# Kernel tuning notes

Measured on AMD Instinct MI355X. Metric: run time of the kernel, lower is better.

The kernel has to match this reference:

```python
import jax, jax.numpy as jnp
import numpy as np

N_NODES = 50000
F_DIM = 256
D_EMB = 128
R_REL = 3
N_PICK = 4096
K_NEIGH = 32


def _dist_score(x, w1, b1, w2, b2):
    # distance_net: Linear(F,16) -> ReLU -> Linear(16,2) -> Sigmoid; take class-1 column
    h = jax.nn.relu(x @ w1 + b1)
    return jax.nn.sigmoid(h @ w2 + b2)[..., 1]


def setup_inputs() -> dict:
    key = jax.random.key(0)
    ks = jax.random.split(key, 10)
    return {
        "features": jax.random.normal(ks[0], (N_NODES, F_DIM), dtype=jnp.float32),
        "weight": jax.random.normal(ks[1], (D_EMB, F_DIM), dtype=jnp.float32) * (1.0 / np.sqrt(F_DIM)),
        "W1": jax.random.normal(ks[2], (R_REL, F_DIM, 16), dtype=jnp.float32) * (1.0 / np.sqrt(F_DIM)),
        "b1": jax.random.normal(ks[3], (R_REL, 16), dtype=jnp.float32) * 0.01,
        "W2": jax.random.normal(ks[4], (R_REL, 16, 2), dtype=jnp.float32) * 0.25,
        "b2": jax.random.normal(ks[5], (R_REL, 2), dtype=jnp.float32) * 0.01,
        "picked_nodes": jax.random.randint(ks[6], (R_REL, N_PICK), 0, N_NODES),
        "picked_labels": jax.random.randint(ks[7], (R_REL, N_PICK), 0, 2),
        "neigh_idx": jax.random.randint(ks[8], (R_REL, N_PICK, K_NEIGH), 0, N_NODES),
        "cand_idx": jax.random.randint(ks[9], (R_REL, N_PICK, K_NEIGH), 0, N_NODES),
    }


def reference(features, weight, W1, b1, W2, b2, picked_nodes, picked_labels, neigh_idx, cand_idx):
    R, n = picked_nodes.shape
    K = neigh_idx.shape[-1]
    dt = features.dtype
    agg = jnp.zeros((n, features.shape[1]), dtype=dt)  # [n, F]
    triu = jnp.triu(jnp.ones((n, n), dtype=dt), 1)
    for r in range(R):  # small fixed relation loop (structurally distinct params)
        lab = picked_labels[r]
        feats_r = features[picked_nodes[r]]                       # [n, F]
        d = _dist_score(feats_r, W1[r], b1[r], W2[r], b2[r])      # [n]
        # ----- rho_plus: top-K mean of pairwise |d_a - d_b| among minority-class nodes -----
        n_pos = jnp.sum(lab)
        minority = jnp.where(n_pos <= n - n_pos, 1, 0)
        minmask = (lab == minority).astype(dt)                    # [n]
        pair = jnp.abs(d[:, None] - d[None, :])                   # [n, n]
        valid = minmask[:, None] * minmask[None, :] * triu
        masked = jnp.where(valid > 0, pair, -1.0)
        top_plus, _ = jax.lax.top_k(masked.reshape(-1), K)        # avg neighborhood size ~ K
        rho_plus = jnp.mean(jnp.maximum(top_plus, 0.0))
        # ----- rho_minus: top n/2 mean of |d_v - d_u| over graph neighbors -----
        nfeat = features[neigh_idx[r]]                            # [n, K, F]
        d_nb = _dist_score(nfeat, W1[r], b1[r], W2[r], b2[r])     # [n, K]
        diff_nb = jnp.abs(d[:, None] - d_nb)                      # [n, K]
        top_minus, _ = jax.lax.top_k(diff_nb.reshape(-1), n // 2)
        rho_minus = jnp.mean(top_minus)
        # ----- gather neighbor features where distance diff below thresholds -----
        m_minus = (diff_nb < rho_minus).astype(dt)                # [n, K]
        cfeat = features[cand_idx[r]]                             # [n, K, F] same-label candidates
        d_cd = _dist_score(cfeat, W1[r], b1[r], W2[r], b2[r])     # [n, K]
        m_plus = (jnp.abs(d[:, None] - d_cd) < rho_plus).astype(dt)
        agg = agg + jnp.einsum('nk,nkf->nf', m_minus, nfeat) + jnp.einsum('nk,nkf->nf', m_plus, cfeat)
    center = features[picked_nodes[0]]                            # [n, F] center batch
    center_h = weight @ center.T                                  # [D, n]
    neigh_h = weight @ agg.T                                      # [D, n]
    return jax.nn.relu(center_h + neigh_h)                        # [D, n]
```

## Files before the change

kernel.cpp:

```cpp
#include <hip/hip_runtime.h>
#include <math.h>

#define NN 50000
#define FD 256
#define DE 128
#define RR 3
#define NP 4096
#define KN 32

#define OFF_DPICK 0
#define OFF_DNB   12288
#define OFF_DCD   405504
#define OFF_RHOM  798720
#define OFF_RHOP  798724
#define OFF_DALL  798976
#define OFF_AGG   798976
#define OFF_HIST  948976
#define OFF_STATE 955120
#define OFF_PSUM  955128
#define OFF_PCNT  955224

__device__ __forceinline__ int wave_red_int(int v) {
    #pragma unroll
    for (int o = 1; o < 64; o <<= 1) v += __shfl_xor(v, o);
    return v;
}
__device__ __forceinline__ double wave_red_dbl(double v) {
    #pragma unroll
    for (int o = 1; o < 64; o <<= 1) v += __shfl_xor(v, o);
    return v;
}

__device__ unsigned kth_bits(const float* arr, int L, int K,
                             int (*cnt_sh)[16], unsigned* x_sh_p) {
    const int tid = threadIdx.x, lane = tid & 63, wv = tid >> 6;
    unsigned x = 0;
    for (int b = 27; b >= 0; b -= 3) {
        int cnt[7];
        #pragma unroll
        for (int q = 0; q < 7; ++q) cnt[q] = 0;
        for (int i = tid; i < L; i += 1024) {
            unsigned vb = __float_as_uint(arr[i]);
            #pragma unroll
            for (int q = 0; q < 7; ++q) cnt[q] += (vb >= (x | ((unsigned)(q + 1) << b)));
        }
        #pragma unroll
        for (int q = 0; q < 7; ++q) cnt[q] = wave_red_int(cnt[q]);
        if (lane == 0) {
            #pragma unroll
            for (int q = 0; q < 7; ++q) cnt_sh[q][wv] = cnt[q];
        }
        __syncthreads();
        if (tid == 0) {
            unsigned nx = x;
            for (int q = 6; q >= 0; --q) {
                int tot = 0;
                for (int w = 0; w < 16; ++w) tot += cnt_sh[q][w];
                if (tot >= K) { nx = x | ((unsigned)(q + 1) << b); break; }
            }
            *x_sh_p = nx;
        }
        __syncthreads();
        x = *x_sh_p;
        __syncthreads();
    }
    return x;
}

__global__ __launch_bounds__(256, 4) void dall_kernel(
    const float* __restrict__ features,
    const float* __restrict__ W1, const float* __restrict__ b1,
    const float* __restrict__ W2, const float* __restrict__ b2,
    float* ws)
{
    const int r = blockIdx.y;
    const int wid = blockIdx.x * 4 + (threadIdx.x >> 6);
    const int lane = threadIdx.x & 63;
    const int s = lane >> 4, j = lane & 15;
    const int base = wid * 32;
    if (base >= NN) return;

    float w1f[64];
    const float* W1r = W1 + r * (FD * 16);
    #pragma unroll
    for (int tt = 0; tt < 64; ++tt) w1f[tt] = W1r[(s * 64 + tt) * 16 + j];
    const float b1v = b1[r * 16 + j];
    const float w2v = W2[(r * 16 + j) * 2 + 1];
    const float b2v = b2[r * 2 + 1];

    float res = 0.f;
    #pragma unroll 2
    for (int i = 0; i < 32; ++i) {
        const int node = min(base + i, NN - 1);
        const float4* x4 = (const float4*)(features + (long)node * FD);
        float acc = 0.f;
        #pragma unroll
        for (int t4 = 0; t4 < 16; ++t4) {
            float4 xv = x4[s * 16 + t4];
            acc = fmaf(xv.x, w1f[4 * t4 + 0], acc);
            acc = fmaf(xv.y, w1f[4 * t4 + 1], acc);
            acc = fmaf(xv.z, w1f[4 * t4 + 2], acc);
            acc = fmaf(xv.w, w1f[4 * t4 + 3], acc);
        }
        acc += __shfl_xor(acc, 16);
        acc += __shfl_xor(acc, 32);
        float h = fmaxf(acc + b1v, 0.f);
        float p = h * w2v;
        p += __shfl_xor(p, 1);
        p += __shfl_xor(p, 2);
        p += __shfl_xor(p, 4);
        p += __shfl_xor(p, 8);
        if (lane == i) res = p;
    }
    const int node = base + lane;
    if (lane < 32 && node < NN)
        ws[OFF_DALL + r * NN + node] = 1.f / (1.f + expf(-(res + b2v)));
}

__global__ __launch_bounds__(256) void gather_kernel(
    const int* __restrict__ picked, const int* __restrict__ neigh,
    const int* __restrict__ cand, float* ws)
{
    const int t = blockIdx.x * 256 + threadIdx.x;
    const float* dall = ws + OFF_DALL;
    if (t < 6144) ((int*)(ws + OFF_HIST))[t] = 0;
    else if (t < 6150) {
        int* st = (int*)(ws + OFF_STATE);
        if (t < 6147) st[t - 6144] = 0;
        else          st[t - 6147 + 3] = NP / 2;
    }
    if (t < RR * NP) {
        const int r = t >> 12;
        ws[OFF_DPICK + t] = dall[r * NN + picked[t]];
    } else if (t < RR * NP + RR * NP * KN) {
        const int off = t - RR * NP;
        const int r = off >> 17;
        const int n = (off >> 5) & (NP - 1);
        const float dp = dall[r * NN + picked[r * NP + n]];
        ws[OFF_DNB + off] = fabsf(dp - dall[r * NN + neigh[off]]);
    } else {
        const int off = t - RR * NP - RR * NP * KN;
        const int r = off >> 17;
        const int n = (off >> 5) & (NP - 1);
        const float dp = dall[r * NN + picked[r * NP + n]];
        ws[OFF_DCD + off] = fabsf(dp - dall[r * NN + cand[off]]);
    }
}

__global__ __launch_bounds__(256) void rho_hist_kernel(float* ws, int pass)
{
    __shared__ int h[4][2048];
    const int tid = threadIdx.x, wv = tid >> 6;
    const int r = blockIdx.y;
    for (int i = tid; i < 8192; i += 256) ((int*)h)[i] = 0;
    __syncthreads();

    const int* st = (const int*)(ws + OFF_STATE);
    const unsigned prefix = (unsigned)st[r];
    const float* __restrict__ dnb = ws + OFF_DNB + r * (NP * KN);
    const int base = blockIdx.x * 8192;
    #pragma unroll 4
    for (int k = 0; k < 32; ++k) {
        unsigned vb = __float_as_uint(dnb[base + k * 256 + tid]);
        int bin; bool ok;
        if (pass == 0)      { bin = vb >> 21;           ok = true; }
        else if (pass == 1) { bin = (vb >> 10) & 0x7FF; ok = ((vb >> 21) == prefix); }
        else                { bin = vb & 0x3FF;         ok = ((vb >> 10) == prefix); }
        if (ok) atomicAdd(&h[wv][bin], 1);
    }
    __syncthreads();
    int* hist = (int*)(ws + OFF_HIST) + r * 2048;
    for (int b = tid; b < 2048; b += 256) {
        int s = h[0][b] + h[1][b] + h[2][b] + h[3][b];
        if (s) atomicAdd(&hist[b], s);
    }
}

__global__ __launch_bounds__(1024) void rho_select_kernel(float* ws, int pass)
{
    __shared__ int s0[2048], s1[2048];
    const int tid = threadIdx.x;
    const int r = blockIdx.x;
    int* hist = (int*)(ws + OFF_HIST) + r * 2048;
    int* st = (int*)(ws + OFF_STATE);

    s0[tid] = hist[tid]; s0[tid + 1024] = hist[tid + 1024];
    __syncthreads();
    int* src = s0; int* dst = s1;
    for (int off = 1; off < 2048; off <<= 1) {
        for (int i = tid; i < 2048; i += 1024) {
            int v = src[i];
            if (i + off < 2048) v += src[i + off];
            dst[i] = v;
        }
        __syncthreads();
        int* tmp = src; src = dst; dst = tmp;
    }
    const int remK = st[3 + r];
    for (int i = tid; i < 2048; i += 1024) {
        const int sfx = src[i];
        const int nxt = (i < 2047) ? src[i + 1] : 0;
        if (sfx >= remK && nxt < remK) {
            const unsigned prefix = (unsigned)st[r];
            st[r] = (pass == 0) ? i
                  : (pass == 1) ? (int)((prefix << 11) | (unsigned)i)
                                : (int)((prefix << 10) | (unsigned)i);
            st[3 + r] = remK - nxt;
        }
        hist[i] = 0;
    }
}

__global__ __launch_bounds__(256) void rho_sum_kernel(float* ws)
{
    __shared__ double ds[4];
    __shared__ int    is[4];
    const int tid = threadIdx.x, lane = tid & 63, wv = tid >> 6;
    const int r = blockIdx.y;
    const unsigned x = (unsigned)((const int*)(ws + OFF_STATE))[r];
    const float* __restrict__ dnb = ws + OFF_DNB + r * (NP * KN);
    const int base = blockIdx.x * 8192;
    double s = 0.0; int c = 0;
    #pragma unroll 4
    for (int k = 0; k < 32; ++k) {
        float v = dnb[base + k * 256 + tid];
        if (__float_as_uint(v) > x) { s += (double)v; c += 1; }
    }
    s = wave_red_dbl(s); c = wave_red_int(c);
    if (lane == 0) { ds[wv] = s; is[wv] = c; }
    __syncthreads();
    if (tid == 0) {
        double st = ds[0] + ds[1] + ds[2] + ds[3];
        int ct = is[0] + is[1] + is[2] + is[3];
        ((double*)(ws + OFF_PSUM))[r * 16 + blockIdx.x] = st;
        ((int*)(ws + OFF_PCNT))[r * 16 + blockIdx.x] = ct;
    }
}

__global__ __launch_bounds__(1024) void rho_plus_kernel(float* ws, const int* __restrict__ labels)
{
    __shared__ float cv[2048];
    __shared__ float cnd[2048];
    __shared__ float tvb[64];
    __shared__ int   cnt_sh[7][16];
    __shared__ int   ired[16];
    __shared__ double dred[16];
    __shared__ int   m_sh, npos_sh, cnt2_sh;
    __shared__ unsigned x_sh;

    const int tid = threadIdx.x;
    const int lane = tid & 63, wv = tid >> 6;
    const int r = blockIdx.x;

    if (tid == 0) {
        const double* psum = (const double*)(ws + OFF_PSUM);
        const int* pcnt = (const int*)(ws + OFF_PCNT);
        double tot = 0; int cg = 0;
        for (int i = 0; i < 16; ++i) { tot += psum[r * 16 + i]; cg += pcnt[r * 16 + i]; }
        const unsigned x = (unsigned)((const int*)(ws + OFF_STATE))[r];
        tot += (double)(NP / 2 - cg) * (double)__uint_as_float(x);
        ws[OFF_RHOM + r] = (float)(tot / (double)(NP / 2));
    }

    const float* dpr = ws + OFF_DPICK + r * NP;
    const int* lab = labels + r * NP;
    int np = 0;
    for (int i = tid; i < NP; i += 1024) np += lab[i];
    np = wave_red_int(np);
    if (lane == 0) ired[wv] = np;
    __syncthreads();
    if (tid == 0) {
        int sacc = 0;
        for (int w = 0; w < 16; ++w) sacc += ired[w];
        npos_sh = sacc; m_sh = 0;
    }
    __syncthreads();
    const int minority = (2 * npos_sh <= NP) ? 1 : 0;
    for (int i = tid; i < NP; i += 1024) {
        bool pred = (lab[i] == minority);
        unsigned long long bal = __ballot(pred);
        int wcnt = __popcll(bal);
        int woff = __popcll(bal & ((1ull << lane) - 1ull));
        int bb = 0;
        if (lane == 0 && wcnt) bb = atomicAdd(&m_sh, wcnt);
        bb = __shfl(bb, 0);
        if (pred) cv[bb + woff] = dpr[i];
    }
    __syncthreads();
    const int m = m_sh;

    if (m >= 64) {
        const unsigned thi = kth_bits(cv, m, 32, cnt_sh, &x_sh);
        if (tid == 0) cnt2_sh = 0;
        __syncthreads();
        for (int i = tid; i < m; i += 1024) {
            bool pred = __float_as_uint(cv[i]) > thi;
            unsigned long long bal = __ballot(pred);
            int wcnt = __popcll(bal);
            int woff = __popcll(bal & ((1ull << lane) - 1ull));
            int bb = 0;
            if (lane == 0 && wcnt) bb = atomicAdd(&cnt2_sh, wcnt);
            bb = __shfl(bb, 0);
            if (pred) tvb[bb + woff] = cv[i];
        }
        __syncthreads();
        if (tid < 32 && tid >= cnt2_sh) tvb[tid] = __uint_as_float(thi);
        __syncthreads();
        const unsigned tlo = kth_bits(cv, m, m - 31, cnt_sh, &x_sh);
        if (tid == 0) cnt2_sh = 0;
        __syncthreads();
        for (int i = tid; i < m; i += 1024) {
            bool pred = __float_as_uint(cv[i]) < tlo;
            unsigned long long bal = __ballot(pred);
            int wcnt = __popcll(bal);
            int woff = __popcll(bal & ((1ull << lane) - 1ull));
            int bb = 0;
            if (lane == 0 && wcnt) bb = atomicAdd(&cnt2_sh, wcnt);
            bb = __shfl(bb, 0);
            if (pred) tvb[32 + bb + woff] = cv[i];
        }
        __syncthreads();
        if (tid < 32 && tid >= cnt2_sh) tvb[32 + tid] = __uint_as_float(tlo);
        __syncthreads();
        cnd[tid] = tvb[tid >> 5] - tvb[32 + (tid & 31)];
        cnd[tid + 1024] = 0.0f;
    } else {
        cnd[tid] = 0.0f; cnd[tid + 1024] = 0.0f;
        __syncthreads();
        int idx = 0;
        for (int a = 0; a + 1 < m; ++a)
            for (int bq = a + 1; bq < m; ++bq) {
                if ((idx & 1023) == tid) cnd[idx] = fabsf(cv[a] - cv[bq]);
                ++idx;
            }
    }
    __syncthreads();
    const unsigned tc = kth_bits(cnd, 2048, 32, cnt_sh, &x_sh);
    double ps = 0.0; int pc = 0;
    {
        float v = cnd[tid];
        if (__float_as_uint(v) > tc) { ps += (double)v; pc += 1; }
        v = cnd[tid + 1024];
        if (__float_as_uint(v) > tc) { ps += (double)v; pc += 1; }
    }
    ps = wave_red_dbl(ps); pc = wave_red_int(pc);
    if (lane == 0) { dred[wv] = ps; ired[wv] = pc; }
    __syncthreads();
    if (tid == 0) {
        double tot = 0; int cg = 0;
        for (int w = 0; w < 16; ++w) { tot += dred[w]; cg += ired[w]; }
        tot += (double)(32 - cg) * (double)__uint_as_float(tc);
        ws[OFF_RHOP + r] = (float)(tot / 32.0);
    }
}

__global__ __launch_bounds__(256) void agg_kernel(
    const float* __restrict__ features,
    const int* __restrict__ picked, const int* __restrict__ neigh,
    const int* __restrict__ cndi, float* ws)
{
    __shared__ float4 sacc[2][64];
    const int wvid = threadIdx.x >> 6;
    const int half = wvid & 1;
    const int pair = wvid >> 1;
    const int n = __builtin_amdgcn_readfirstlane(blockIdx.x * 2 + pair);
    const int lane = threadIdx.x & 63;
    const float4* f4 = (const float4*)features;

    float4 acc = {0.f, 0.f, 0.f, 0.f};
    if (half == 0) acc = f4[(long)picked[n] * 64 + lane];
    const int* __restrict__ isrc = half ? cndi : neigh;
    const float* dsrc = ws + (half ? OFF_DCD : OFF_DNB);
    #pragma unroll
    for (int r = 0; r < RR; ++r) {
        const float rho = ws[(half ? OFF_RHOP : OFF_RHOM) + r];
        const int base = (r * NP + n) * KN;
        const int   id = isrc[base + (lane & 31)];
        const float dv = dsrc[base + (lane & 31)];
        unsigned long long bal = __ballot(dv < rho);
        const unsigned msk = (unsigned)bal;
        #pragma unroll
        for (int c = 0; c < 4; ++c) {
            float4 v[8];
            #pragma unroll
            for (int q = 0; q < 8; ++q) {
                int node = __shfl(id, c * 8 + q);
                v[q] = f4[(long)node * 64 + lane];
            }
            #pragma unroll
            for (int q = 0; q < 8; ++q) {
                float mfl = ((msk >> (c * 8 + q)) & 1) ? 1.f : 0.f;
                acc.x = fmaf(v[q].x, mfl, acc.x);
                acc.y = fmaf(v[q].y, mfl, acc.y);
                acc.z = fmaf(v[q].z, mfl, acc.z);
                acc.w = fmaf(v[q].w, mfl, acc.w);
            }
        }
    }
    if (half == 1) sacc[pair][lane] = acc;
    __syncthreads();
    if (half == 0) {
        float4 o = sacc[pair][lane];
        acc.x += o.x; acc.y += o.y; acc.z += o.z; acc.w += o.w;
        float4* agg4 = (float4*)(ws + OFF_AGG);
        agg4[(long)n * 64 + lane] = acc;
    }
}

__global__ __launch_bounds__(256) void gemm_kernel(
    const float* __restrict__ weight, const float* ws, float* __restrict__ out)
{
    __shared__ __align__(16) float sW[32 * 256];
    __shared__ float sA[32 * 257];
    const int t = threadIdx.x;
    const int nt = blockIdx.x, dt = blockIdx.y;
    const float* agg = ws + OFF_AGG;

    const float4* w4 = (const float4*)(weight + dt * (32 * 256));
    float4* sW4 = (float4*)sW;
    #pragma unroll
    for (int i = 0; i < 8; ++i) sW4[i * 256 + t] = w4[i * 256 + t];

    const float4* a4 = (const float4*)agg + (long)nt * 2048;
    #pragma unroll
    for (int i = 0; i < 8; ++i) {
        int f4i = i * 256 + t;
        float4 v = a4[f4i];
        int row = f4i >> 6, c0 = (f4i & 63) << 2;
        sA[row * 257 + c0 + 0] = v.x;
        sA[row * 257 + c0 + 1] = v.y;
        sA[row * 257 + c0 + 2] = v.z;
        sA[row * 257 + c0 + 3] = v.w;
    }
    __syncthreads();

    const int n = t & 31, g = t >> 5;
    const float* sAn = sA + n * 257;
    const float* sWg = sW + g * (4 * 256);
    float acc[4] = {0.f, 0.f, 0.f, 0.f};
    for (int c4 = 0; c4 < 64; ++c4) {
        float a0 = sAn[c4 * 4 + 0], a1 = sAn[c4 * 4 + 1];
        float a2 = sAn[c4 * 4 + 2], a3 = sAn[c4 * 4 + 3];
        #pragma unroll
        for (int i = 0; i < 4; ++i) {
            const float4 wvv = *(const float4*)(sWg + i * 256 + c4 * 4);
            acc[i] = fmaf(wvv.x, a0, acc[i]);
            acc[i] = fmaf(wvv.y, a1, acc[i]);
            acc[i] = fmaf(wvv.z, a2, acc[i]);
            acc[i] = fmaf(wvv.w, a3, acc[i]);
        }
    }
    float* outp = out + (long)(dt * 32 + g * 4) * 4096 + nt * 32 + n;
    #pragma unroll
    for (int i = 0; i < 4; ++i) outp[(long)i * 4096] = fmaxf(acc[i], 0.f);
}

extern "C" void kernel_launch(void* const* d_in, const int* in_sizes, int n_in,
                              void* d_out, int out_size, void* d_ws, size_t ws_size,
                              hipStream_t stream)
{
    const float* features = (const float*)d_in[0];
    const float* weight   = (const float*)d_in[1];
    const float* W1       = (const float*)d_in[2];
    const float* b1       = (const float*)d_in[3];
    const float* W2       = (const float*)d_in[4];
    const float* b2       = (const float*)d_in[5];
    const int*   picked   = (const int*)d_in[6];
    const int*   labels   = (const int*)d_in[7];
    const int*   neigh    = (const int*)d_in[8];
    const int*   cnd      = (const int*)d_in[9];
    float* out = (float*)d_out;
    float* ws  = (float*)d_ws;

    dall_kernel<<<dim3(391, 3), 256, 0, stream>>>(features, W1, b1, W2, b2, ws);
    gather_kernel<<<3120, 256, 0, stream>>>(picked, neigh, cnd, ws);
    rho_hist_kernel<<<dim3(16, 3), 256, 0, stream>>>(ws, 0);
    rho_select_kernel<<<3, 1024, 0, stream>>>(ws, 0);
    rho_hist_kernel<<<dim3(16, 3), 256, 0, stream>>>(ws, 1);
    rho_select_kernel<<<3, 1024, 0, stream>>>(ws, 1);
    rho_hist_kernel<<<dim3(16, 3), 256, 0, stream>>>(ws, 2);
    rho_select_kernel<<<3, 1024, 0, stream>>>(ws, 2);
    rho_sum_kernel<<<dim3(16, 3), 256, 0, stream>>>(ws);
    rho_plus_kernel<<<3, 1024, 0, stream>>>(ws, labels);
    agg_kernel<<<2048, 256, 0, stream>>>(features, picked, neigh, cnd, ws);
    gemm_kernel<<<dim3(128, 4), 256, 0, stream>>>(weight, ws, out);
}
```

Before: 440.2 us.

## Stage features in LDS, emit fp16 copy, and gather fp16 in aggregation

The distance-score kernel now loads each 32-node tile of features into shared memory once and computes all three relations from it, instead of re-reading features per relation. When the workspace is large enough, it also writes an fp16 copy of the features, and the aggregation kernel gathers neighbor and candidate rows from that copy to halve gather traffic. The separate rho_sum kernel is folded into rho_plus, which now scans the whole neighbor-diff array in a single block per relation. Risks are reduced accuracy in the aggregated sums, extra write traffic for the fp16 copy, and a serialized reduction in rho_plus.

After: 384.8 us. 1.14x faster.

```diff
diff --git a/kernel.cpp b/kernel.cpp
--- a/kernel.cpp
+++ b/kernel.cpp
@@ -1,4 +1,5 @@
 #include <hip/hip_runtime.h>
+#include <hip/hip_fp16.h>
 #include <math.h>
 
 #define NN 50000
@@ -17,8 +18,8 @@
 #define OFF_AGG   798976
 #define OFF_HIST  948976
 #define OFF_STATE 955120
-#define OFF_PSUM  955128
-#define OFF_PCNT  955224
+#define OFF_F16   1847552
+#define WS_NEED_F16 33000000ull
 
 __device__ __forceinline__ int wave_red_int(int v) {
     #pragma unroll
@@ -67,18 +68,40 @@
     return x;
 }
 
-__global__ __launch_bounds__(256, 4) void dall_kernel(
+__global__ __launch_bounds__(384) void dall_kernel(
     const float* __restrict__ features,
     const float* __restrict__ W1, const float* __restrict__ b1,
     const float* __restrict__ W2, const float* __restrict__ b2,
-    float* ws)
-{
-    const int r = blockIdx.y;
-    const int wid = blockIdx.x * 4 + (threadIdx.x >> 6);
-    const int lane = threadIdx.x & 63;
+    float* ws, int make_f16)
+{
+    __shared__ float xs[32 * 272];
+    const int t = threadIdx.x;
+    const int base = blockIdx.x * 32;
+    unsigned short* bf = (unsigned short*)(ws + OFF_F16);
+
+    #pragma unroll
+    for (int i = 0; i < 6; ++i) {
+        const int idx = i * 384 + t;
+        if (idx < 2048) {
+            const int row = idx >> 6, c4 = idx & 63;
+            const int node = base + row;
+            const float4 v = ((const float4*)features)[(long)min(node, NN - 1) * 64 + c4];
+            *(float4*)&xs[row * 272 + (c4 >> 4) * 68 + (c4 & 15) * 4] = v;
+            if (make_f16 && node < NN) {
+                ushort4 hv;
+                hv.x = __half_as_ushort(__float2half(v.x));
+                hv.y = __half_as_ushort(__float2half(v.y));
+                hv.z = __half_as_ushort(__float2half(v.z));
+                hv.w = __half_as_ushort(__float2half(v.w));
+                ((ushort4*)bf)[(long)node * 64 + c4] = hv;
+            }
+        }
+    }
+    __syncthreads();
+
+    const int wv = t >> 6, lane = t & 63;
+    const int r = wv >> 1, half = wv & 1;
     const int s = lane >> 4, j = lane & 15;
-    const int base = wid * 32;
-    if (base >= NN) return;
 
     float w1f[64];
     const float* W1r = W1 + r * (FD * 16);
@@ -89,14 +112,13 @@
     const float b2v = b2[r * 2 + 1];
 
     float res = 0.f;
-    #pragma unroll 2
-    for (int i = 0; i < 32; ++i) {
-        const int node = min(base + i, NN - 1);
-        const float4* x4 = (const float4*)(features + (long)node * FD);
+    #pragma unroll 4
+    for (int i = 0; i < 16; ++i) {
+        const float* xp = &xs[(half * 16 + i) * 272 + s * 68];
         float acc = 0.f;
         #pragma unroll
         for (int t4 = 0; t4 < 16; ++t4) {
-            float4 xv = x4[s * 16 + t4];
+            const float4 xv = *(const float4*)(xp + t4 * 4);
             acc = fmaf(xv.x, w1f[4 * t4 + 0], acc);
             acc = fmaf(xv.y, w1f[4 * t4 + 1], acc);
             acc = fmaf(xv.z, w1f[4 * t4 + 2], acc);
@@ -112,8 +134,8 @@
         p += __shfl_xor(p, 8);
         if (lane == i) res = p;
     }
-    const int node = base + lane;
-    if (lane < 32 && node < NN)
+    const int node = base + half * 16 + lane;
+    if (lane < 16 && node < NN)
         ws[OFF_DALL + r * NN + node] = 1.f / (1.f + expf(-(res + b2v)));
 }
 
@@ -211,32 +233,6 @@
     }
 }
 
-__global__ __launch_bounds__(256) void rho_sum_kernel(float* ws)
-{
-    __shared__ double ds[4];
-    __shared__ int    is[4];
-    const int tid = threadIdx.x, lane = tid & 63, wv = tid >> 6;
-    const int r = blockIdx.y;
-    const unsigned x = (unsigned)((const int*)(ws + OFF_STATE))[r];
-    const float* __restrict__ dnb = ws + OFF_DNB + r * (NP * KN);
-    const int base = blockIdx.x * 8192;
-    double s = 0.0; int c = 0;
-    #pragma unroll 4
-    for (int k = 0; k < 32; ++k) {
-        float v = dnb[base + k * 256 + tid];
-        if (__float_as_uint(v) > x) { s += (double)v; c += 1; }
-    }
-    s = wave_red_dbl(s); c = wave_red_int(c);
-    if (lane == 0) { ds[wv] = s; is[wv] = c; }
-    __syncthreads();
-    if (tid == 0) {
-        double st = ds[0] + ds[1] + ds[2] + ds[3];
-        int ct = is[0] + is[1] + is[2] + is[3];
-        ((double*)(ws + OFF_PSUM))[r * 16 + blockIdx.x] = st;
-        ((int*)(ws + OFF_PCNT))[r * 16 + blockIdx.x] = ct;
-    }
-}
-
 __global__ __launch_bounds__(1024) void rho_plus_kernel(float* ws, const int* __restrict__ labels)
 {
     __shared__ float cv[2048];
@@ -252,14 +248,24 @@
     const int lane = tid & 63, wv = tid >> 6;
     const int r = blockIdx.x;
 
-    if (tid == 0) {
-        const double* psum = (const double*)(ws + OFF_PSUM);
-        const int* pcnt = (const int*)(ws + OFF_PCNT);
-        double tot = 0; int cg = 0;
-        for (int i = 0; i < 16; ++i) { tot += psum[r * 16 + i]; cg += pcnt[r * 16 + i]; }
+    {
         const unsigned x = (unsigned)((const int*)(ws + OFF_STATE))[r];
-        tot += (double)(NP / 2 - cg) * (double)__uint_as_float(x);
-        ws[OFF_RHOM + r] = (float)(tot / (double)(NP / 2));
+        const float* __restrict__ dnb = ws + OFF_DNB + r * (NP * KN);
+        double ps = 0.0; int pc = 0;
+        for (int i = tid; i < NP * KN; i += 1024) {
+            float v = dnb[i];
+            if (__float_as_uint(v) > x) { ps += (double)v; pc += 1; }
+        }
+        ps = wave_red_dbl(ps); pc = wave_red_int(pc);
+        if (lane == 0) { dred[wv] = ps; ired[wv] = pc; }
+        __syncthreads();
+        if (tid == 0) {
+            double tot = 0; int cg = 0;
+            for (int w = 0; w < 16; ++w) { tot += dred[w]; cg += ired[w]; }
+            tot += (double)(NP / 2 - cg) * (double)__uint_as_float(x);
+            ws[OFF_RHOM + r] = (float)(tot / (double)(NP / 2));
+        }
+        __syncthreads();
     }
 
     const float* dpr = ws + OFF_DPICK + r * NP;
@@ -354,7 +360,61 @@
     }
 }
 
-__global__ __launch_bounds__(256) void agg_kernel(
+__global__ __launch_bounds__(256) void agg_kernel_f16(
+    const float* __restrict__ features,
+    const int* __restrict__ picked, const int* __restrict__ neigh,
+    const int* __restrict__ cndi, float* ws)
+{
+    __shared__ float4 sacc[2][64];
+    const int wvid = threadIdx.x >> 6;
+    const int half = wvid & 1;
+    const int pair = wvid >> 1;
+    const int n = __builtin_amdgcn_readfirstlane(blockIdx.x * 2 + pair);
+    const int lane = threadIdx.x & 63;
+    const float4* f4 = (const float4*)features;
+    const ushort4* h4 = (const ushort4*)(ws + OFF_F16);
+
+    float4 acc = {0.f, 0.f, 0.f, 0.f};
+    if (half == 0) acc = f4[(long)picked[n] * 64 + lane];
+    const int* __restrict__ isrc = half ? cndi : neigh;
+    const float* dsrc = ws + (half ? OFF_DCD : OFF_DNB);
+    #pragma unroll
+    for (int r = 0; r < RR; ++r) {
+        const float rho = ws[(half ? OFF_RHOP : OFF_RHOM) + r];
+        const int base = (r * NP + n) * KN;
+        const int   id = isrc[base + (lane & 31)];
+        const float dv = dsrc[base + (lane & 31)];
+        unsigned long long bal = __ballot(dv < rho);
+        const unsigned msk = (unsigned)bal;
+        #pragma unroll
+        for (int c = 0; c < 2; ++c) {
+            ushort4 v[16];
+            #pragma unroll
+            for (int q = 0; q < 16; ++q) {
+                int node = __shfl(id, c * 16 + q);
+                v[q] = h4[(long)node * 64 + lane];
+            }
+            #pragma unroll
+            for (int q = 0; q < 16; ++q) {
+                float mfl = ((msk >> (c * 16 + q)) & 1) ? 1.f : 0.f;
+                acc.x = fmaf(__half2float(__ushort_as_half(v[q].x)), mfl, acc.x);
+                acc.y = fmaf(__half2float(__ushort_as_half(v[q].y)), mfl, acc.y);
+                acc.z = fmaf(__half2float(__ushort_as_half(v[q].z)), mfl, acc.z);
+                acc.w = fmaf(__half2float(__ushort_as_half(v[q].w)), mfl, acc.w);
+            }
+        }
+    }
+    if (half == 1) sacc[pair][lane] = acc;
+    __syncthreads();
+    if (half == 0) {
+        float4 o = sacc[pair][lane];
+        acc.x += o.x; acc.y += o.y; acc.z += o.z; acc.w += o.w;
+        float4* agg4 = (float4*)(ws + OFF_AGG);
+        agg4[(long)n * 64 + lane] = acc;
+    }
+}
+
+__global__ __launch_bounds__(256) void agg_kernel_f32(
     const float* __restrict__ features,
     const int* __restrict__ picked, const int* __restrict__ neigh,
     const int* __restrict__ cndi, float* ws)
@@ -472,7 +532,9 @@
     float* out = (float*)d_out;
     float* ws  = (float*)d_ws;
 
-    dall_kernel<<<dim3(391, 3), 256, 0, stream>>>(features, W1, b1, W2, b2, ws);
+    const int use_f16 = (ws_size >= WS_NEED_F16) ? 1 : 0;
+
+    dall_kernel<<<1563, 384, 0, stream>>>(features, W1, b1, W2, b2, ws, use_f16);
     gather_kernel<<<3120, 256, 0, stream>>>(picked, neigh, cnd, ws);
     rho_hist_kernel<<<dim3(16, 3), 256, 0, stream>>>(ws, 0);
     rho_select_kernel<<<3, 1024, 0, stream>>>(ws, 0);
@@ -480,8 +542,10 @@
     rho_select_kernel<<<3, 1024, 0, stream>>>(ws, 1);
     rho_hist_kernel<<<dim3(16, 3), 256, 0, stream>>>(ws, 2);
     rho_select_kernel<<<3, 1024, 0, stream>>>(ws, 2);
-    rho_sum_kernel<<<dim3(16, 3), 256, 0, stream>>>(ws);
     rho_plus_kernel<<<3, 1024, 0, stream>>>(ws, labels);
-    agg_kernel<<<2048, 256, 0, stream>>>(features, picked, neigh, cnd, ws);
+    if (use_f16)
+        agg_kernel_f16<<<2048, 256, 0, stream>>>(features, picked, neigh, cnd, ws);
+    else
+        agg_kernel_f32<<<2048, 256, 0, stream>>>(features, picked, neigh, cnd, ws);
     gemm_kernel<<<dim3(128, 4), 256, 0, stream>>>(weight, ws, out);
 }
```
